# Kernel optimization log

Measured on AMD Instinct MI355X. Metric: run time of the kernel, lower is better.

Reference implementation:

```python
import jax, jax.numpy as jnp
import numpy as np

B, M, T, D, V = 16, 1024, 4096, 512, 32000
HOPS = 2  # multi_layer_gcn layer_number=2


def setup_inputs() -> dict:
    key = jax.random.key(0)
    ks = jax.random.split(key, 10)
    s = 1.0 / np.sqrt(D)
    emb = jax.random.normal(ks[0], (V, D), jnp.float32) * 0.02
    Ws = jax.random.normal(ks[1], (HOPS, D, D), jnp.float32) * s
    Wn = jax.random.normal(ks[2], (HOPS, D, D), jnp.float32) * s
    Wr = jax.random.normal(ks[3], (HOPS, D, D), jnp.float32) * s
    Wt = jax.random.normal(ks[4], (D, 3 * D), jnp.float32) * (1.0 / np.sqrt(3 * D))
    concept_ids = jax.random.randint(ks[5], (B, M), 0, V)
    relation = jax.random.randint(ks[6], (B, T), 0, V)
    head = jax.random.randint(ks[7], (B, T), 0, M)
    tail = jax.random.randint(ks[8], (B, T), 0, M)
    triple_label = jax.random.randint(ks[9], (B, T), -1, 2)  # {-1,0,1}
    return dict(emb=emb, Ws=Ws, Wn=Wn, Wr=Wr, Wt=Wt,
                concept_ids=concept_ids, relation=relation,
                head=head, tail=tail, triple_label=triple_label)


def _forward(emb, Ws, Wn, Wr, Wt, concept_ids, relation, head, tail, triple_label):
    x = emb[concept_ids]        # [B, M, D] node hidden
    rel = emb[relation]         # [B, T, D] relation hidden
    mask = (triple_label != -1).astype(x.dtype)  # [B, T]

    # per-batch scatter_add into M node slots
    scat = jax.vmap(lambda msg, idx: jnp.zeros((M, msg.shape[-1]), msg.dtype).at[idx].add(msg))
    scat1 = jax.vmap(lambda v, idx: jnp.zeros((M,), v.dtype).at[idx].add(v))

    for i in range(HOPS):
        oh = jnp.take_along_axis(x, head[..., None], axis=1) * mask[..., None]  # gather heads
        ot = jnp.take_along_axis(x, tail[..., None], axis=1) * mask[..., None]  # gather tails
        relm = rel * mask[..., None]
        # update_node += scatter(head_repr - rel -> tail) + scatter(tail_repr - rel -> head)
        upd = scat(oh - relm, tail) + scat(ot - relm, head)          # [B, M, D]
        cnt = scat1(mask, tail) + scat1(mask, head)                  # [B, M]
        x = jax.nn.relu(
            jnp.einsum('bmd,ed->bme', x, Ws[i])
            + jnp.einsum('bmd,ed->bme', upd, Wn[i]) / jnp.maximum(cnt, 1.0)[..., None]
        )
        rel = jnp.einsum('btd,ed->bte', rel, Wr[i])

    head_repr = jnp.take_along_axis(x, head[..., None], axis=1)  # [B, T, D]
    tail_repr = jnp.take_along_axis(x, tail[..., None], axis=1)  # [B, T, D]
    triple_repr = jnp.concatenate([head_repr, rel, tail_repr], axis=-1)  # [B, T, 3D]
    triple_repr = jnp.einsum('btk,dk->btd', triple_repr, Wt)     # [B, T, D]
    encoded_cause = triple_repr.sum(axis=1)                      # [B, D]
    return triple_repr, encoded_cause


def reference(emb, Ws, Wn, Wr, Wt, concept_ids, relation, head, tail, triple_label):
    return _forward(emb, Ws, Wn, Wr, Wt, concept_ids, relation, head, tail, triple_label)
```

## Files before the change

### kernel.cpp

```cpp
#include <hip/hip_runtime.h>

namespace {

constexpr int kB = 16;
constexpr int kM = 1024;
constexpr int kT = 4096;
constexpr int kD = 512;
constexpr int kV = 32000;

typedef __attribute__((ext_vector_type(8))) short bfrag8;
typedef __attribute__((ext_vector_type(4))) float f4acc;

__device__ __forceinline__ ushort f2bf(float f) {
  unsigned u = __float_as_uint(f);
  u += 0x7fffu + ((u >> 16) & 1u);
  return (ushort)(u >> 16);
}
__device__ __forceinline__ float bf2f(ushort h) {
  return __uint_as_float(((unsigned)h) << 16);
}

__device__ __forceinline__ void gload_lds16(const void* g, void* l) {
  __builtin_amdgcn_global_load_lds(
      (const __attribute__((address_space(1))) void*)g,
      (__attribute__((address_space(3))) void*)l, 16, 0, 0);
}

constexpr int kN0 = kV * kD / 4;
constexpr int kN1 = kN0 + 2 * kD * kD / 4;
constexpr int kN2 = kN1 + 2 * kD * kD / 4;
constexpr int kN3 = kN2 + kD * 1536 / 4;
constexpr int kN4 = kN3 + kB * kM * 128;

__global__ __launch_bounds__(256) void prep_k(
    const float4* __restrict__ emb, const float4* __restrict__ Ws,
    const float4* __restrict__ Wn, const float4* __restrict__ Wt,
    const int* __restrict__ cid,
    ushort4* __restrict__ EMBb, ushort4* __restrict__ Wsb,
    ushort4* __restrict__ Wnb, ushort4* __restrict__ Wtb,
    ushort4* __restrict__ X0)
{
  int i = blockIdx.x * 256 + threadIdx.x;
  if (i >= kN4) return;
  const float4* s;
  ushort4* d;
  int off;
  if (i < kN0) { s = emb; d = EMBb; off = i; }
  else if (i < kN1) { s = Ws; d = Wsb; off = i - kN0; }
  else if (i < kN2) { s = Wn; d = Wnb; off = i - kN1; }
  else if (i < kN3) { s = Wt; d = Wtb; off = i - kN2; }
  else {
    int idx = i - kN3;
    int row = idx >> 7;
    int c = idx & 127;
    float4 v = emb[(size_t)cid[row] * 128 + c];
    ushort4 o;
    o.x = f2bf(v.x); o.y = f2bf(v.y); o.z = f2bf(v.z); o.w = f2bf(v.w);
    X0[idx] = o;
    return;
  }
  float4 v = s[off];
  ushort4 o;
  o.x = f2bf(v.x); o.y = f2bf(v.y); o.z = f2bf(v.z); o.w = f2bf(v.w);
  d[off] = o;
}

__global__ __launch_bounds__(512) void smallmm2_k(
    const float* __restrict__ Wn, const float* __restrict__ Wt,
    const float* __restrict__ Wr,
    ushort* __restrict__ Wn2r, float* __restrict__ T1)
{
  __shared__ float prow[4][512];
  const int job = blockIdx.x >> 7;
  const int e0 = (blockIdx.x & 127) * 4;
  const int k = threadIdx.x;
  const float* P;
  int strideP, offsP;
  const float* Q;
  if (job == 0) { P = Wn + (size_t)kD * kD; strideP = 512; offsP = 0; Q = Wr; }
  else { P = Wt; strideP = 1536; offsP = 512; Q = Wr + (size_t)kD * kD; }
#pragma unroll
  for (int i = 0; i < 4; ++i)
    prow[i][k] = P[(size_t)(e0 + i) * strideP + offsP + k];
  __syncthreads();
  float acc[4] = {0.f, 0.f, 0.f, 0.f};
  for (int a = 0; a < 512; ++a) {
    float qv = Q[a * 512 + k];
#pragma unroll
    for (int i = 0; i < 4; ++i) acc[i] = fmaf(prow[i][a], qv, acc[i]);
  }
#pragma unroll
  for (int i = 0; i < 4; ++i) {
    if (job == 0) Wn2r[(e0 + i) * 512 + k] = f2bf(acc[i]);
    else T1[(e0 + i) * 512 + k] = acc[i];
  }
}

__global__ __launch_bounds__(512) void smallmm_k(
    const float* __restrict__ P, const float* __restrict__ Q,
    ushort* __restrict__ outb)
{
  __shared__ float prow[4][512];
  int e0 = blockIdx.x * 4;
  int k = threadIdx.x;
#pragma unroll
  for (int i = 0; i < 4; ++i)
    prow[i][k] = P[(size_t)(e0 + i) * 512 + k];
  __syncthreads();
  float acc[4] = {0.f, 0.f, 0.f, 0.f};
  for (int a = 0; a < 512; ++a) {
    float qv = Q[a * 512 + k];
#pragma unroll
    for (int i = 0; i < 4; ++i) acc[i] = fmaf(prow[i][a], qv, acc[i]);
  }
#pragma unroll
  for (int i = 0; i < 4; ++i) outb[(e0 + i) * 512 + k] = f2bf(acc[i]);
}

__global__ __launch_bounds__(1024) void csr_k(
    const int* __restrict__ headp, const int* __restrict__ tailp,
    const int* __restrict__ lblp,
    int* __restrict__ deg, int* __restrict__ rowstart,
    int* __restrict__ epack)
{
  __shared__ int sdeg[kM];
  __shared__ int sscan[kM];
  __shared__ int sfill[kM];
  const int b = blockIdx.x;
  const int tid = threadIdx.x;
  sdeg[tid] = 0;
  __syncthreads();
  const int* hb = headp + (b << 12);
  const int* tb = tailp + (b << 12);
  const int* lb = lblp + (b << 12);
  for (int t = tid; t < kT; t += 1024) {
    if (lb[t] == -1) continue;
    atomicAdd(&sdeg[tb[t]], 1);
    atomicAdd(&sdeg[hb[t]], 1);
  }
  __syncthreads();
  int d = sdeg[tid];
  sscan[tid] = d;
  __syncthreads();
  for (int off = 1; off < kM; off <<= 1) {
    int add = (tid >= off) ? sscan[tid - off] : 0;
    __syncthreads();
    sscan[tid] += add;
    __syncthreads();
  }
  int rs = b * (2 * kT) + sscan[tid] - d;
  deg[(b << 10) + tid] = d;
  rowstart[(b << 10) + tid] = rs;
  sfill[tid] = rs;
  __syncthreads();
  for (int t = tid; t < kT; t += 1024) {
    if (lb[t] == -1) continue;
    int hd = hb[t];
    int tl = tb[t];
    int p0 = atomicAdd(&sfill[tl], 1);
    epack[p0] = ((t * 2) << 10) | hd;
    int p1 = atomicAdd(&sfill[hd], 1);
    epack[p1] = ((t * 2 + 1) << 10) | tl;
  }
  __syncthreads();
  for (int i = 1; i < d; ++i) {
    int key = epack[rs + i];
    int j = i - 1;
    while (j >= 0 && epack[rs + j] > key) {
      epack[rs + j + 1] = epack[rs + j];
      --j;
    }
    epack[rs + j + 1] = key;
  }
}

__global__ __launch_bounds__(128) void agg_xr_k(
    const ushort4* __restrict__ Xv, const ushort4* __restrict__ EMBv,
    const int* __restrict__ relid,
    const int* __restrict__ deg, const int* __restrict__ rowstart,
    const int* __restrict__ epack,
    ushort4* __restrict__ Sxn, ushort4* __restrict__ nSr0n)
{
  int bm = blockIdx.x;
  int b = bm >> 10;
  int tid = threadIdx.x;
  int dg = deg[bm];
  int rs = rowstart[bm];
  const int* rid = relid + (b << 12);
  size_t xbase = (size_t)b * kM * 128;
  float ax = 0.f, ay = 0.f, az = 0.f, aw = 0.f;
  float rx = 0.f, ry = 0.f, rz = 0.f, rw = 0.f;
  int e = 0;
  for (; e + 4 <= dg; e += 4) {
    int pk[4];
#pragma unroll
    for (int j = 0; j < 4; ++j) pk[j] = epack[rs + e + j];
    ushort4 xv[4], rv[4];
#pragma unroll
    for (int j = 0; j < 4; ++j) {
      xv[j] = Xv[xbase + (size_t)(pk[j] & 1023) * 128 + tid];
      rv[j] = EMBv[(size_t)rid[pk[j] >> 11] * 128 + tid];
    }
#pragma unroll
    for (int j = 0; j < 4; ++j) {
      ax += bf2f(xv[j].x); ay += bf2f(xv[j].y);
      az += bf2f(xv[j].z); aw += bf2f(xv[j].w);
      rx += bf2f(rv[j].x); ry += bf2f(rv[j].y);
      rz += bf2f(rv[j].z); rw += bf2f(rv[j].w);
    }
  }
  for (; e < dg; ++e) {
    int pk = epack[rs + e];
    ushort4 xv = Xv[xbase + (size_t)(pk & 1023) * 128 + tid];
    ushort4 rv = EMBv[(size_t)rid[pk >> 11] * 128 + tid];
    ax += bf2f(xv.x); ay += bf2f(xv.y); az += bf2f(xv.z); aw += bf2f(xv.w);
    rx += bf2f(rv.x); ry += bf2f(rv.y); rz += bf2f(rv.z); rw += bf2f(rv.w);
  }
  float s = 1.0f / (float)(dg > 0 ? dg : 1);
  ushort4 o;
  o.x = f2bf(ax * s); o.y = f2bf(ay * s); o.z = f2bf(az * s); o.w = f2bf(aw * s);
  Sxn[(size_t)bm * 128 + tid] = o;
  o.x = f2bf(-rx * s); o.y = f2bf(-ry * s);
  o.z = f2bf(-rz * s); o.w = f2bf(-rw * s);
  nSr0n[(size_t)bm * 128 + tid] = o;
}

__global__ __launch_bounds__(128) void agg_x_k(
    const ushort4* __restrict__ Xv,
    const int* __restrict__ deg, const int* __restrict__ rowstart,
    const int* __restrict__ epack, ushort4* __restrict__ outv)
{
  int bm = blockIdx.x;
  int b = bm >> 10;
  int tid = threadIdx.x;
  int dg = deg[bm];
  int rs = rowstart[bm];
  size_t xbase = (size_t)b * kM * 128;
  float ax = 0.f, ay = 0.f, az = 0.f, aw = 0.f;
  int e = 0;
  for (; e + 4 <= dg; e += 4) {
    int pk[4];
#pragma unroll
    for (int j = 0; j < 4; ++j) pk[j] = epack[rs + e + j];
    ushort4 xv[4];
#pragma unroll
    for (int j = 0; j < 4; ++j)
      xv[j] = Xv[xbase + (size_t)(pk[j] & 1023) * 128 + tid];
#pragma unroll
    for (int j = 0; j < 4; ++j) {
      ax += bf2f(xv[j].x); ay += bf2f(xv[j].y);
      az += bf2f(xv[j].z); aw += bf2f(xv[j].w);
    }
  }
  for (; e < dg; ++e) {
    int src = epack[rs + e] & 1023;
    ushort4 xv = Xv[xbase + (size_t)src * 128 + tid];
    ax += bf2f(xv.x); ay += bf2f(xv.y); az += bf2f(xv.z); aw += bf2f(xv.w);
  }
  float s = 1.0f / (float)(dg > 0 ? dg : 1);
  ushort4 o;
  o.x = f2bf(ax * s); o.y = f2bf(ay * s); o.z = f2bf(az * s); o.w = f2bf(aw * s);
  outv[(size_t)bm * 128 + tid] = o;
}

template<int MODE>
__global__ __launch_bounds__(256) void gemm_k(
    const ushort* __restrict__ A0, const ushort* __restrict__ A1,
    const ushort* __restrict__ A2,
    const ushort* __restrict__ W1, const ushort* __restrict__ W2,
    const ushort* __restrict__ W3,
    ushort* __restrict__ outbf)
{
  constexpr int NSEG = (MODE == 0) ? 3 : 1;
  constexpr int NC = (MODE == 4) ? 8 : 4;
  constexpr int OSTR = (MODE == 4) ? 1024 : 512;
  constexpr bool SWZ = (MODE != 5);

  __shared__ __align__(16) char lds[32768];
  char* ldsA = lds;
  char* ldsB = lds + 16384;
  const int tid = threadIdx.x;
  const int w = tid >> 6;
  const int l = tid & 63;
  const int wr = w >> 1;
  const int wc = w & 1;
  const int bid = blockIdx.x;
  int panel, col;
  if constexpr (SWZ) {
    int xcd = bid & 7;
    int idx = bid >> 3;
    panel = xcd * (((int)gridDim.x >> 3) / NC) + idx / NC;
    col = idx % NC;
  } else {
    panel = bid >> 2;
    col = bid & 3;
  }
  const int rowBase = panel * 128;
  const int colBase = col * 128;

  f4acc acc[4][4];
#pragma unroll
  for (int i = 0; i < 4; ++i)
#pragma unroll
    for (int j = 0; j < 4; ++j) acc[i][j] = (f4acc)(0.f);

  int lrow[4], gc[4];
#pragma unroll
  for (int i = 0; i < 4; ++i) {
    int P = (i * 4 + w) * 64 + l;
    lrow[i] = P >> 3;
    gc[i] = (P & 7) ^ (lrow[i] & 7);
  }

  for (int seg = 0; seg < NSEG; ++seg) {
    const char* aP[4];
    const char* bP[4];
#pragma unroll
    for (int i = 0; i < 4; ++i) {
      int grow = rowBase + lrow[i];
      const ushort* ab;
      if constexpr (MODE == 0) {
        ab = (seg == 0 ? A0 : (seg == 1 ? A1 : A2)) + (size_t)grow * kD;
      } else {
        ab = A0 + (size_t)grow * kD;
      }
      aP[i] = (const char*)ab + gc[i] * 16;
      int e = colBase + lrow[i];
      const ushort* wb;
      if constexpr (MODE == 0) {
        wb = (seg == 0 ? W1 : (seg == 1 ? W2 : W3)) + (size_t)e * kD;
      } else if constexpr (MODE == 4) {
        wb = W1 + (size_t)(e & 511) * 1536 + (e >> 9) * 1024;
      } else {
        wb = W1 + (size_t)e * kD;
      }
      bP[i] = (const char*)wb + gc[i] * 16;
    }
    for (int kcl = 0; kcl < 8; ++kcl) {
      __syncthreads();
#pragma unroll
      for (int i = 0; i < 4; ++i) {
        gload_lds16(aP[i] + kcl * 128, ldsA + (i * 4 + w) * 1024);
        gload_lds16(bP[i] + kcl * 128, ldsB + (i * 4 + w) * 1024);
      }
      __syncthreads();
#pragma unroll
      for (int ksub = 0; ksub < 2; ++ksub) {
        bfrag8 ef[4], wf[4];
#pragma unroll
        for (int mi = 0; mi < 4; ++mi) {
          int r = wr * 64 + mi * 16 + (l & 15);
          int g = (ksub * 4 + (l >> 4)) ^ (r & 7);
          ef[mi] = *(const bfrag8*)(ldsA + r * 128 + g * 16);
        }
#pragma unroll
        for (int ni = 0; ni < 4; ++ni) {
          int e = wc * 64 + ni * 16 + (l & 15);
          int g = (ksub * 4 + (l >> 4)) ^ (e & 7);
          wf[ni] = *(const bfrag8*)(ldsB + e * 128 + g * 16);
        }
#pragma unroll
        for (int mi = 0; mi < 4; ++mi)
#pragma unroll
          for (int ni = 0; ni < 4; ++ni)
            acc[mi][ni] = __builtin_amdgcn_mfma_f32_16x16x32_bf16(
                wf[ni], ef[mi], acc[mi][ni], 0, 0, 0);
      }
    }
  }

#pragma unroll
  for (int mi = 0; mi < 4; ++mi) {
    int rr = rowBase + wr * 64 + mi * 16 + (l & 15);
#pragma unroll
    for (int ni = 0; ni < 4; ++ni) {
      int cc0 = colBase + wc * 64 + ni * 16 + (l >> 4) * 4;
      float v0 = acc[mi][ni][0], v1 = acc[mi][ni][1];
      float v2 = acc[mi][ni][2], v3 = acc[mi][ni][3];
      if constexpr (MODE == 0) {
        v0 = fmaxf(v0, 0.f); v1 = fmaxf(v1, 0.f);
        v2 = fmaxf(v2, 0.f); v3 = fmaxf(v3, 0.f);
      }
      ushort4 o;
      o.x = f2bf(v0); o.y = f2bf(v1); o.z = f2bf(v2); o.w = f2bf(v3);
      *(ushort4*)(outbf + (size_t)rr * OSTR + cc0) = o;
    }
  }
}

__global__ __launch_bounds__(128) void final_add_k(
    const ushort4* __restrict__ REL2v, const ushort4* __restrict__ HTv,
    const int* __restrict__ relid, const int* __restrict__ headp,
    const int* __restrict__ tailp,
    float* __restrict__ outf, float* __restrict__ part)
{
  const int blk = blockIdx.x;
  const int tid = threadIdx.x;
  const int r0 = blk * 32;
  float cs0 = 0.f, cs1 = 0.f, cs2 = 0.f, cs3 = 0.f;
  for (int i = 0; i < 32; i += 8) {
    ushort4 rv[8], hv[8], tv[8];
#pragma unroll
    for (int j = 0; j < 8; ++j) {
      int r = r0 + i + j;
      int bb = r >> 12;
      rv[j] = REL2v[(size_t)relid[r] * 128 + tid];
      hv[j] = HTv[((size_t)(bb << 10) + headp[r]) * 256 + tid];
      tv[j] = HTv[((size_t)(bb << 10) + tailp[r]) * 256 + 128 + tid];
    }
#pragma unroll
    for (int j = 0; j < 8; ++j) {
      float4 ov;
      ov.x = bf2f(rv[j].x) + bf2f(hv[j].x) + bf2f(tv[j].x);
      ov.y = bf2f(rv[j].y) + bf2f(hv[j].y) + bf2f(tv[j].y);
      ov.z = bf2f(rv[j].z) + bf2f(hv[j].z) + bf2f(tv[j].z);
      ov.w = bf2f(rv[j].w) + bf2f(hv[j].w) + bf2f(tv[j].w);
      cs0 += ov.x; cs1 += ov.y; cs2 += ov.z; cs3 += ov.w;
      *(float4*)(outf + (size_t)(r0 + i + j) * 512 + tid * 4) = ov;
    }
  }
  float4 o; o.x = cs0; o.y = cs1; o.z = cs2; o.w = cs3;
  *(float4*)(part + (size_t)blk * 512 + tid * 4) = o;
}

__global__ __launch_bounds__(512) void reduce_enc_k(
    const float* __restrict__ part, float* __restrict__ enc)
{
  int b = blockIdx.x;
  int c = threadIdx.x;
  float s = 0.f;
  for (int rt = 0; rt < 128; ++rt) s += part[(size_t)(b * 128 + rt) * 512 + c];
  enc[b * 512 + c] = s;
}

}

extern "C" void kernel_launch(void* const* d_in, const int* in_sizes, int n_in,
                              void* d_out, int out_size, void* d_ws, size_t ws_size,
                              hipStream_t stream) {
  const float* emb = (const float*)d_in[0];
  const float* Ws = (const float*)d_in[1];
  const float* Wn = (const float*)d_in[2];
  const float* Wr = (const float*)d_in[3];
  const float* Wt = (const float*)d_in[4];
  const int* cid = (const int*)d_in[5];
  const int* relid = (const int*)d_in[6];
  const int* headp = (const int*)d_in[7];
  const int* tailp = (const int*)d_in[8];
  const int* lblp = (const int*)d_in[9];
  float* out = (float*)d_out;

  char* wsp = (char*)d_ws;
  ushort* EMBb  = (ushort*)(wsp);
  ushort* HT    = (ushort*)(wsp);
  ushort* REL2  = (ushort*)(wsp + (32ull << 20));
  ushort* Wsb   = (ushort*)(wsp + (64ull << 20));
  ushort* Wnb   = (ushort*)(wsp + (65ull << 20));
  ushort* Wtb   = (ushort*)(wsp + (66ull << 20));
  ushort* Wn2r  = (ushort*)(wsp + (67ull << 20) + (512ull << 10));
  ushort* Wfold = (ushort*)(wsp + (68ull << 20));
  float*  T1    = (float*)(wsp + (68ull << 20) + (512ull << 10));
  int* deg      = (int*)(wsp + (70ull << 20));
  int* rowstart = deg + kB * kM;
  int* epack    = rowstart + kB * kM;
  float* part   = (float*)(wsp + (71ull << 20));

  char* outc = (char*)d_out;
  ushort* X      = (ushort*)(outc);
  ushort* Sxn    = (ushort*)(outc + (16ull << 20));
  ushort* nSr0n  = (ushort*)(outc + (32ull << 20));
  float* ENC = out + (size_t)kB * kT * kD;

  prep_k<<<(kN4 + 255) / 256, 256, 0, stream>>>(
      (const float4*)emb, (const float4*)Ws, (const float4*)Wn,
      (const float4*)Wt, cid, (ushort4*)EMBb, (ushort4*)Wsb, (ushort4*)Wnb,
      (ushort4*)Wtb, (ushort4*)X);

  smallmm2_k<<<256, 512, 0, stream>>>(Wn, Wt, Wr, Wn2r, T1);
  smallmm_k<<<128, 512, 0, stream>>>(T1, Wr, Wfold);

  csr_k<<<kB, 1024, 0, stream>>>(headp, tailp, lblp, deg, rowstart, epack);

  agg_xr_k<<<kB * kM, 128, 0, stream>>>(
      (const ushort4*)X, (const ushort4*)EMBb, relid, deg, rowstart, epack,
      (ushort4*)Sxn, (ushort4*)nSr0n);

  gemm_k<0><<<(kB * kM / 128) * 4, 256, 0, stream>>>(
      X, Sxn, nSr0n, Wsb, Wnb, Wnb, X);

  gemm_k<5><<<(kV / 128) * 4, 256, 0, stream>>>(
      EMBb, nullptr, nullptr, Wfold, nullptr, nullptr, REL2);

  agg_x_k<<<kB * kM, 128, 0, stream>>>(
      (const ushort4*)X, deg, rowstart, epack, (ushort4*)Sxn);

  gemm_k<0><<<(kB * kM / 128) * 4, 256, 0, stream>>>(
      X, Sxn, nSr0n, Wsb + (size_t)kD * kD, Wnb + (size_t)kD * kD, Wn2r, X);

  gemm_k<4><<<(kB * kM / 128) * 8, 256, 0, stream>>>(
      X, nullptr, nullptr, Wtb, nullptr, nullptr, HT);

  final_add_k<<<kB * kT / 32, 128, 0, stream>>>(
      (const ushort4*)REL2, (const ushort4*)HT, relid, headp, tailp, out, part);

  reduce_enc_k<<<kB, 512, 0, stream>>>(part, ENC);
}
```

Measured before the change: 317.4 us.

## Fuse prep, CSR and weight-product kernels; fold hop-1 relation term into aggregate

Merges the bf16 conversion, CSR build and small weight-product kernels into one launch, with work routed by block index. The Wfold product is merged with the first aggregation kernel, which now packs four nodes per 512-thread block. The first hop's relation aggregate is subtracted from the node aggregate before the GEMM, so the layer-0 GEMM drops from three K segments to two (new MODE 1). X now ping-pongs between separate buffers, so no GEMM writes into the array it reads. This saves launches and one third of the first-layer GEMM work, at the cost of extra bf16 rounding on the combined aggregate and uneven block workloads inside the fused kernels.

```diff
diff --git a/kernel.cpp b/kernel.cpp
--- a/kernel.cpp
+++ b/kernel.cpp
@@ -31,198 +31,208 @@
 constexpr int kN2 = kN1 + 2 * kD * kD / 4;
 constexpr int kN3 = kN2 + kD * 1536 / 4;
 constexpr int kN4 = kN3 + kB * kM * 128;
-
-__global__ __launch_bounds__(256) void prep_k(
+constexpr int kPREPB = kN4 / 1024;
+constexpr int kCSRB = 16;
+constexpr int kMM2B = 256;
+
+__global__ __launch_bounds__(1024) void fused_prep_k(
     const float4* __restrict__ emb, const float4* __restrict__ Ws,
     const float4* __restrict__ Wn, const float4* __restrict__ Wt,
+    const float* __restrict__ Wnf, const float* __restrict__ Wtf,
+    const float* __restrict__ Wrf,
     const int* __restrict__ cid,
+    const int* __restrict__ headp, const int* __restrict__ tailp,
+    const int* __restrict__ lblp,
     ushort4* __restrict__ EMBb, ushort4* __restrict__ Wsb,
     ushort4* __restrict__ Wnb, ushort4* __restrict__ Wtb,
-    ushort4* __restrict__ X0)
+    ushort4* __restrict__ X0,
+    int* __restrict__ deg, int* __restrict__ rowstart, int* __restrict__ epack,
+    ushort* __restrict__ Wn2r, float* __restrict__ T1)
 {
-  int i = blockIdx.x * 256 + threadIdx.x;
-  if (i >= kN4) return;
-  const float4* s;
-  ushort4* d;
-  int off;
-  if (i < kN0) { s = emb; d = EMBb; off = i; }
-  else if (i < kN1) { s = Ws; d = Wsb; off = i - kN0; }
-  else if (i < kN2) { s = Wn; d = Wnb; off = i - kN1; }
-  else if (i < kN3) { s = Wt; d = Wtb; off = i - kN2; }
-  else {
-    int idx = i - kN3;
-    int row = idx >> 7;
-    int c = idx & 127;
-    float4 v = emb[(size_t)cid[row] * 128 + c];
+  __shared__ __align__(16) char shm[12288];
+  const int bid = blockIdx.x;
+  const int tid = threadIdx.x;
+
+  if (bid < kCSRB) {
+    int* sdeg = (int*)shm;
+    int* sscan = (int*)(shm + 4096);
+    int* sfill = (int*)(shm + 8192);
+    const int b = bid;
+    sdeg[tid] = 0;
+    __syncthreads();
+    const int* hb = headp + (b << 12);
+    const int* tb = tailp + (b << 12);
+    const int* lb = lblp + (b << 12);
+    for (int t = tid; t < kT; t += 1024) {
+      if (lb[t] == -1) continue;
+      atomicAdd(&sdeg[tb[t]], 1);
+      atomicAdd(&sdeg[hb[t]], 1);
+    }
+    __syncthreads();
+    int d = sdeg[tid];
+    sscan[tid] = d;
+    __syncthreads();
+    for (int off = 1; off < kM; off <<= 1) {
+      int add = (tid >= off) ? sscan[tid - off] : 0;
+      __syncthreads();
+      sscan[tid] += add;
+      __syncthreads();
+    }
+    int rs = b * (2 * kT) + sscan[tid] - d;
+    deg[(b << 10) + tid] = d;
+    rowstart[(b << 10) + tid] = rs;
+    sfill[tid] = rs;
+    __syncthreads();
+    for (int t = tid; t < kT; t += 1024) {
+      if (lb[t] == -1) continue;
+      int hd = hb[t];
+      int tl = tb[t];
+      int p0 = atomicAdd(&sfill[tl], 1);
+      epack[p0] = ((t * 2) << 10) | hd;
+      int p1 = atomicAdd(&sfill[hd], 1);
+      epack[p1] = ((t * 2 + 1) << 10) | tl;
+    }
+    __syncthreads();
+    for (int i = 1; i < d; ++i) {
+      int key = epack[rs + i];
+      int j = i - 1;
+      while (j >= 0 && epack[rs + j] > key) {
+        epack[rs + j + 1] = epack[rs + j];
+        --j;
+      }
+      epack[rs + j + 1] = key;
+    }
+  } else if (bid < kCSRB + kPREPB) {
+    int i = (bid - kCSRB) * 1024 + tid;
+    if (i >= kN4) return;
+    const float4* s;
+    ushort4* dP;
+    int off;
+    if (i < kN0) { s = emb; dP = EMBb; off = i; }
+    else if (i < kN1) { s = Ws; dP = Wsb; off = i - kN0; }
+    else if (i < kN2) { s = Wn; dP = Wnb; off = i - kN1; }
+    else if (i < kN3) { s = Wt; dP = Wtb; off = i - kN2; }
+    else {
+      int idx = i - kN3;
+      int row = idx >> 7;
+      int c = idx & 127;
+      float4 v = emb[(size_t)cid[row] * 128 + c];
+      ushort4 o;
+      o.x = f2bf(v.x); o.y = f2bf(v.y); o.z = f2bf(v.z); o.w = f2bf(v.w);
+      X0[idx] = o;
+      return;
+    }
+    float4 v = s[off];
     ushort4 o;
     o.x = f2bf(v.x); o.y = f2bf(v.y); o.z = f2bf(v.z); o.w = f2bf(v.w);
-    X0[idx] = o;
-    return;
-  }
-  float4 v = s[off];
-  ushort4 o;
-  o.x = f2bf(v.x); o.y = f2bf(v.y); o.z = f2bf(v.z); o.w = f2bf(v.w);
-  d[off] = o;
-}
-
-__global__ __launch_bounds__(512) void smallmm2_k(
-    const float* __restrict__ Wn, const float* __restrict__ Wt,
-    const float* __restrict__ Wr,
-    ushort* __restrict__ Wn2r, float* __restrict__ T1)
-{
-  __shared__ float prow[4][512];
-  const int job = blockIdx.x >> 7;
-  const int e0 = (blockIdx.x & 127) * 4;
-  const int k = threadIdx.x;
-  const float* P;
-  int strideP, offsP;
-  const float* Q;
-  if (job == 0) { P = Wn + (size_t)kD * kD; strideP = 512; offsP = 0; Q = Wr; }
-  else { P = Wt; strideP = 1536; offsP = 512; Q = Wr + (size_t)kD * kD; }
-#pragma unroll
-  for (int i = 0; i < 4; ++i)
-    prow[i][k] = P[(size_t)(e0 + i) * strideP + offsP + k];
-  __syncthreads();
-  float acc[4] = {0.f, 0.f, 0.f, 0.f};
-  for (int a = 0; a < 512; ++a) {
-    float qv = Q[a * 512 + k];
-#pragma unroll
-    for (int i = 0; i < 4; ++i) acc[i] = fmaf(prow[i][a], qv, acc[i]);
-  }
-#pragma unroll
-  for (int i = 0; i < 4; ++i) {
-    if (job == 0) Wn2r[(e0 + i) * 512 + k] = f2bf(acc[i]);
-    else T1[(e0 + i) * 512 + k] = acc[i];
-  }
-}
-
-__global__ __launch_bounds__(512) void smallmm_k(
-    const float* __restrict__ P, const float* __restrict__ Q,
-    ushort* __restrict__ outb)
-{
-  __shared__ float prow[4][512];
-  int e0 = blockIdx.x * 4;
-  int k = threadIdx.x;
-#pragma unroll
-  for (int i = 0; i < 4; ++i)
-    prow[i][k] = P[(size_t)(e0 + i) * 512 + k];
-  __syncthreads();
-  float acc[4] = {0.f, 0.f, 0.f, 0.f};
-  for (int a = 0; a < 512; ++a) {
-    float qv = Q[a * 512 + k];
-#pragma unroll
-    for (int i = 0; i < 4; ++i) acc[i] = fmaf(prow[i][a], qv, acc[i]);
-  }
-#pragma unroll
-  for (int i = 0; i < 4; ++i) outb[(e0 + i) * 512 + k] = f2bf(acc[i]);
-}
-
-__global__ __launch_bounds__(1024) void csr_k(
-    const int* __restrict__ headp, const int* __restrict__ tailp,
-    const int* __restrict__ lblp,
-    int* __restrict__ deg, int* __restrict__ rowstart,
-    int* __restrict__ epack)
-{
-  __shared__ int sdeg[kM];
-  __shared__ int sscan[kM];
-  __shared__ int sfill[kM];
-  const int b = blockIdx.x;
-  const int tid = threadIdx.x;
-  sdeg[tid] = 0;
-  __syncthreads();
-  const int* hb = headp + (b << 12);
-  const int* tb = tailp + (b << 12);
-  const int* lb = lblp + (b << 12);
-  for (int t = tid; t < kT; t += 1024) {
-    if (lb[t] == -1) continue;
-    atomicAdd(&sdeg[tb[t]], 1);
-    atomicAdd(&sdeg[hb[t]], 1);
-  }
-  __syncthreads();
-  int d = sdeg[tid];
-  sscan[tid] = d;
-  __syncthreads();
-  for (int off = 1; off < kM; off <<= 1) {
-    int add = (tid >= off) ? sscan[tid - off] : 0;
-    __syncthreads();
-    sscan[tid] += add;
-    __syncthreads();
-  }
-  int rs = b * (2 * kT) + sscan[tid] - d;
-  deg[(b << 10) + tid] = d;
-  rowstart[(b << 10) + tid] = rs;
-  sfill[tid] = rs;
-  __syncthreads();
-  for (int t = tid; t < kT; t += 1024) {
-    if (lb[t] == -1) continue;
-    int hd = hb[t];
-    int tl = tb[t];
-    int p0 = atomicAdd(&sfill[tl], 1);
-    epack[p0] = ((t * 2) << 10) | hd;
-    int p1 = atomicAdd(&sfill[hd], 1);
-    epack[p1] = ((t * 2 + 1) << 10) | tl;
-  }
-  __syncthreads();
-  for (int i = 1; i < d; ++i) {
-    int key = epack[rs + i];
-    int j = i - 1;
-    while (j >= 0 && epack[rs + j] > key) {
-      epack[rs + j + 1] = epack[rs + j];
-      --j;
-    }
-    epack[rs + j + 1] = key;
-  }
-}
-
-__global__ __launch_bounds__(128) void agg_xr_k(
+    dP[off] = o;
+  } else {
+    float (*prow)[512] = (float(*)[512])shm;
+    const int mb = bid - kCSRB - kPREPB;
+    const int job = mb >> 7;
+    const int e0 = (mb & 127) * 4;
+    const int k = tid & 511;
+    const float* P;
+    int strideP, offsP;
+    const float* Q;
+    if (job == 0) { P = Wnf + (size_t)kD * kD; strideP = 512; offsP = 0; Q = Wrf; }
+    else { P = Wtf; strideP = 1536; offsP = 512; Q = Wrf + (size_t)kD * kD; }
+    if (tid < 512) {
+#pragma unroll
+      for (int i = 0; i < 4; ++i)
+        prow[i][k] = P[(size_t)(e0 + i) * strideP + offsP + k];
+    }
+    __syncthreads();
+    if (tid < 512) {
+      float acc[4] = {0.f, 0.f, 0.f, 0.f};
+      for (int a = 0; a < 512; ++a) {
+        float qv = Q[a * 512 + k];
+#pragma unroll
+        for (int i = 0; i < 4; ++i) acc[i] = fmaf(prow[i][a], qv, acc[i]);
+      }
+#pragma unroll
+      for (int i = 0; i < 4; ++i) {
+        if (job == 0) Wn2r[(e0 + i) * 512 + k] = f2bf(acc[i]);
+        else T1[(e0 + i) * 512 + k] = acc[i];
+      }
+    }
+  }
+}
+
+constexpr int kFOLDB = 128;
+
+__global__ __launch_bounds__(512) void fold_aggxr_k(
+    const float* __restrict__ T1, const float* __restrict__ Wrf,
+    ushort* __restrict__ Wfold,
     const ushort4* __restrict__ Xv, const ushort4* __restrict__ EMBv,
     const int* __restrict__ relid,
     const int* __restrict__ deg, const int* __restrict__ rowstart,
     const int* __restrict__ epack,
-    ushort4* __restrict__ Sxn, ushort4* __restrict__ nSr0n)
+    ushort4* __restrict__ SxC, ushort4* __restrict__ nSr0n)
 {
-  int bm = blockIdx.x;
-  int b = bm >> 10;
-  int tid = threadIdx.x;
-  int dg = deg[bm];
-  int rs = rowstart[bm];
-  const int* rid = relid + (b << 12);
-  size_t xbase = (size_t)b * kM * 128;
-  float ax = 0.f, ay = 0.f, az = 0.f, aw = 0.f;
-  float rx = 0.f, ry = 0.f, rz = 0.f, rw = 0.f;
-  int e = 0;
-  for (; e + 4 <= dg; e += 4) {
-    int pk[4];
-#pragma unroll
-    for (int j = 0; j < 4; ++j) pk[j] = epack[rs + e + j];
-    ushort4 xv[4], rv[4];
-#pragma unroll
-    for (int j = 0; j < 4; ++j) {
-      xv[j] = Xv[xbase + (size_t)(pk[j] & 1023) * 128 + tid];
-      rv[j] = EMBv[(size_t)rid[pk[j] >> 11] * 128 + tid];
-    }
-#pragma unroll
-    for (int j = 0; j < 4; ++j) {
-      ax += bf2f(xv[j].x); ay += bf2f(xv[j].y);
-      az += bf2f(xv[j].z); aw += bf2f(xv[j].w);
-      rx += bf2f(rv[j].x); ry += bf2f(rv[j].y);
-      rz += bf2f(rv[j].z); rw += bf2f(rv[j].w);
-    }
-  }
-  for (; e < dg; ++e) {
-    int pk = epack[rs + e];
-    ushort4 xv = Xv[xbase + (size_t)(pk & 1023) * 128 + tid];
-    ushort4 rv = EMBv[(size_t)rid[pk >> 11] * 128 + tid];
-    ax += bf2f(xv.x); ay += bf2f(xv.y); az += bf2f(xv.z); aw += bf2f(xv.w);
-    rx += bf2f(rv.x); ry += bf2f(rv.y); rz += bf2f(rv.z); rw += bf2f(rv.w);
-  }
-  float s = 1.0f / (float)(dg > 0 ? dg : 1);
-  ushort4 o;
-  o.x = f2bf(ax * s); o.y = f2bf(ay * s); o.z = f2bf(az * s); o.w = f2bf(aw * s);
-  Sxn[(size_t)bm * 128 + tid] = o;
-  o.x = f2bf(-rx * s); o.y = f2bf(-ry * s);
-  o.z = f2bf(-rz * s); o.w = f2bf(-rw * s);
-  nSr0n[(size_t)bm * 128 + tid] = o;
+  __shared__ float prow[4][512];
+  const int bid = blockIdx.x;
+  const int tid = threadIdx.x;
+  if (bid < kFOLDB) {
+    int e0 = bid * 4;
+    int k = tid;
+#pragma unroll
+    for (int i = 0; i < 4; ++i)
+      prow[i][k] = T1[(size_t)(e0 + i) * 512 + k];
+    __syncthreads();
+    float acc[4] = {0.f, 0.f, 0.f, 0.f};
+    for (int a = 0; a < 512; ++a) {
+      float qv = Wrf[a * 512 + k];
+#pragma unroll
+      for (int i = 0; i < 4; ++i) acc[i] = fmaf(prow[i][a], qv, acc[i]);
+    }
+#pragma unroll
+    for (int i = 0; i < 4; ++i) Wfold[(e0 + i) * 512 + k] = f2bf(acc[i]);
+  } else {
+    int bm = (bid - kFOLDB) * 4 + (tid >> 7);
+    int t128 = tid & 127;
+    int b = bm >> 10;
+    int dg = deg[bm];
+    int rs = rowstart[bm];
+    const int* rid = relid + (b << 12);
+    size_t xbase = (size_t)b * kM * 128;
+    float ax = 0.f, ay = 0.f, az = 0.f, aw = 0.f;
+    float rx = 0.f, ry = 0.f, rz = 0.f, rw = 0.f;
+    int e = 0;
+    for (; e + 4 <= dg; e += 4) {
+      int pk[4];
+#pragma unroll
+      for (int j = 0; j < 4; ++j) pk[j] = epack[rs + e + j];
+      ushort4 xv[4], rv[4];
+#pragma unroll
+      for (int j = 0; j < 4; ++j) {
+        xv[j] = Xv[xbase + (size_t)(pk[j] & 1023) * 128 + t128];
+        rv[j] = EMBv[(size_t)rid[pk[j] >> 11] * 128 + t128];
+      }
+#pragma unroll
+      for (int j = 0; j < 4; ++j) {
+        ax += bf2f(xv[j].x); ay += bf2f(xv[j].y);
+        az += bf2f(xv[j].z); aw += bf2f(xv[j].w);
+        rx += bf2f(rv[j].x); ry += bf2f(rv[j].y);
+        rz += bf2f(rv[j].z); rw += bf2f(rv[j].w);
+      }
+    }
+    for (; e < dg; ++e) {
+      int pk = epack[rs + e];
+      ushort4 xv = Xv[xbase + (size_t)(pk & 1023) * 128 + t128];
+      ushort4 rv = EMBv[(size_t)rid[pk >> 11] * 128 + t128];
+      ax += bf2f(xv.x); ay += bf2f(xv.y); az += bf2f(xv.z); aw += bf2f(xv.w);
+      rx += bf2f(rv.x); ry += bf2f(rv.y); rz += bf2f(rv.z); rw += bf2f(rv.w);
+    }
+    float s = 1.0f / (float)(dg > 0 ? dg : 1);
+    ushort4 o;
+    o.x = f2bf((ax - rx) * s); o.y = f2bf((ay - ry) * s);
+    o.z = f2bf((az - rz) * s); o.w = f2bf((aw - rw) * s);
+    SxC[(size_t)bm * 128 + t128] = o;
+    o.x = f2bf(-rx * s); o.y = f2bf(-ry * s);
+    o.z = f2bf(-rz * s); o.w = f2bf(-rw * s);
+    nSr0n[(size_t)bm * 128 + t128] = o;
+  }
 }
 
 __global__ __launch_bounds__(128) void agg_x_k(
@@ -271,7 +281,8 @@
     const ushort* __restrict__ W3,
     ushort* __restrict__ outbf)
 {
-  constexpr int NSEG = (MODE == 0) ? 3 : 1;
+  constexpr int NSEG = (MODE == 0) ? 3 : (MODE == 1) ? 2 : 1;
+  constexpr bool RELU = (MODE == 0) || (MODE == 1);
   constexpr int NC = (MODE == 4) ? 8 : 4;
   constexpr int OSTR = (MODE == 4) ? 1024 : 512;
   constexpr bool SWZ = (MODE != 5);
@@ -321,6 +332,8 @@
       const ushort* ab;
       if constexpr (MODE == 0) {
         ab = (seg == 0 ? A0 : (seg == 1 ? A1 : A2)) + (size_t)grow * kD;
+      } else if constexpr (MODE == 1) {
+        ab = (seg == 0 ? A0 : A1) + (size_t)grow * kD;
       } else {
         ab = A0 + (size_t)grow * kD;
       }
@@ -329,6 +342,8 @@
       const ushort* wb;
       if constexpr (MODE == 0) {
         wb = (seg == 0 ? W1 : (seg == 1 ? W2 : W3)) + (size_t)e * kD;
+      } else if constexpr (MODE == 1) {
+        wb = (seg == 0 ? W1 : W2) + (size_t)e * kD;
       } else if constexpr (MODE == 4) {
         wb = W1 + (size_t)(e & 511) * 1536 + (e >> 9) * 1024;
       } else {
@@ -377,7 +392,7 @@
       int cc0 = colBase + wc * 64 + ni * 16 + (l >> 4) * 4;
       float v0 = acc[mi][ni][0], v1 = acc[mi][ni][1];
       float v2 = acc[mi][ni][2], v3 = acc[mi][ni][3];
-      if constexpr (MODE == 0) {
+      if constexpr (RELU) {
         v0 = fmaxf(v0, 0.f); v1 = fmaxf(v1, 0.f);
         v2 = fmaxf(v2, 0.f); v3 = fmaxf(v3, 0.f);
       }
@@ -466,39 +481,37 @@
   float* part   = (float*)(wsp + (71ull << 20));
 
   char* outc = (char*)d_out;
-  ushort* X      = (ushort*)(outc);
-  ushort* Sxn    = (ushort*)(outc + (16ull << 20));
-  ushort* nSr0n  = (ushort*)(outc + (32ull << 20));
+  ushort* X0    = (ushort*)(outc);
+  ushort* Sxn   = (ushort*)(outc + (16ull << 20));
+  ushort* nSr0n = (ushort*)(outc + (32ull << 20));
+  ushort* X1    = (ushort*)(outc + (48ull << 20));
+  ushort* X2    = X0;
   float* ENC = out + (size_t)kB * kT * kD;
 
-  prep_k<<<(kN4 + 255) / 256, 256, 0, stream>>>(
+  fused_prep_k<<<kCSRB + kPREPB + kMM2B, 1024, 0, stream>>>(
       (const float4*)emb, (const float4*)Ws, (const float4*)Wn,
-      (const float4*)Wt, cid, (ushort4*)EMBb, (ushort4*)Wsb, (ushort4*)Wnb,
-      (ushort4*)Wtb, (ushort4*)X);
-
-  smallmm2_k<<<256, 512, 0, stream>>>(Wn, Wt, Wr, Wn2r, T1);
-  smallmm_k<<<128, 512, 0, stream>>>(T1, Wr, Wfold);
-
-  csr_k<<<kB, 1024, 0, stream>>>(headp, tailp, lblp, deg, rowstart, epack);
-
-  agg_xr_k<<<kB * kM, 128, 0, stream>>>(
-      (const ushort4*)X, (const ushort4*)EMBb, relid, deg, rowstart, epack,
-      (ushort4*)Sxn, (ushort4*)nSr0n);
-
-  gemm_k<0><<<(kB * kM / 128) * 4, 256, 0, stream>>>(
-      X, Sxn, nSr0n, Wsb, Wnb, Wnb, X);
+      (const float4*)Wt, Wn, Wt, Wr, cid, headp, tailp, lblp,
+      (ushort4*)EMBb, (ushort4*)Wsb, (ushort4*)Wnb, (ushort4*)Wtb,
+      (ushort4*)X0, deg, rowstart, epack, Wn2r, T1);
+
+  fold_aggxr_k<<<kFOLDB + kB * kM / 4, 512, 0, stream>>>(
+      T1, Wr, Wfold, (const ushort4*)X0, (const ushort4*)EMBb, relid,
+      deg, rowstart, epack, (ushort4*)Sxn, (ushort4*)nSr0n);
+
+  gemm_k<1><<<(kB * kM / 128) * 4, 256, 0, stream>>>(
+      X0, Sxn, nullptr, Wsb, Wnb, nullptr, X1);
 
   gemm_k<5><<<(kV / 128) * 4, 256, 0, stream>>>(
       EMBb, nullptr, nullptr, Wfold, nullptr, nullptr, REL2);
 
   agg_x_k<<<kB * kM, 128, 0, stream>>>(
-      (const ushort4*)X, deg, rowstart, epack, (ushort4*)Sxn);
+      (const ushort4*)X1, deg, rowstart, epack, (ushort4*)Sxn);
 
   gemm_k<0><<<(kB * kM / 128) * 4, 256, 0, stream>>>(
-      X, Sxn, nSr0n, Wsb + (size_t)kD * kD, Wnb + (size_t)kD * kD, Wn2r, X);
+      X1, Sxn, nSr0n, Wsb + (size_t)kD * kD, Wnb + (size_t)kD * kD, Wn2r, X2);
 
   gemm_k<4><<<(kB * kM / 128) * 8, 256, 0, stream>>>(
-      X, nullptr, nullptr, Wtb, nullptr, nullptr, HT);
+      X2, nullptr, nullptr, Wtb, nullptr, nullptr, HT);
 
   final_add_k<<<kB * kT / 32, 128, 0, stream>>>(
       (const ushort4*)REL2, (const ushort4*)HT, relid, headp, tailp, out, part);
```

After: 273.6 us. -13.8%, faster.
